# Optimization experiments

Measured on AMD Instinct MI355X. Metric: run time of the kernel, lower is better.

The kernel has to match this reference:

```python
import jax, jax.numpy as jnp
import numpy as np

D_MODEL, H, D_K, D_V = 512, 8, 64, 64
S_Q, S_KV = 2048, 2048


def setup_inputs() -> dict:
    key = jax.random.key(0)
    ks = jax.random.split(key, 11)
    sc = 0.02
    return {
        "embeddings": jax.random.normal(ks[0], (S_Q, D_MODEL), jnp.float32),
        "K": jax.random.normal(ks[1], (S_KV, D_MODEL), jnp.float32),
        "V": jax.random.normal(ks[2], (S_KV, D_MODEL), jnp.float32),
        # per-head projection weights (stacked over heads) + biases
        "Wq": jax.random.normal(ks[3], (H, D_MODEL, D_K), jnp.float32) * sc,
        "bq": jax.random.normal(ks[4], (H, D_K), jnp.float32) * sc,
        "Wk": jax.random.normal(ks[5], (H, D_MODEL, D_K), jnp.float32) * sc,
        "bk": jax.random.normal(ks[6], (H, D_K), jnp.float32) * sc,
        "Wv": jax.random.normal(ks[7], (H, D_MODEL, D_V), jnp.float32) * sc,
        "bv": jax.random.normal(ks[8], (H, D_V), jnp.float32) * sc,
        # final linear: [h*d_v -> d_model]
        "Wo": jax.random.normal(ks[9], (H * D_V, D_MODEL), jnp.float32) * sc,
        "bo": jax.random.normal(ks[10], (D_MODEL,), jnp.float32) * sc,
    }


def reference(embeddings, K, V, Wq, bq, Wk, bk, Wv, bv, Wo, bo):
    # Batched per-head projections (the original loops over h heads; math identical)
    q = jnp.einsum("sd,hdk->hsk", embeddings, Wq) + bq[:, None, :]  # [h, Sq, d_k]
    k = jnp.einsum("td,hdk->htk", K, Wk) + bk[:, None, :]           # [h, Skv, d_k]
    v = jnp.einsum("td,hdv->htv", V, Wv) + bv[:, None, :]           # [h, Skv, d_v]
    scores = jnp.einsum("hsk,htk->hst", q, k) / jnp.sqrt(jnp.asarray(D_K, q.dtype))
    attn = jax.nn.softmax(scores, axis=-1)                           # [h, Sq, Skv]
    out = jnp.einsum("hst,htv->hsv", attn, v)                        # [h, Sq, d_v]
    # torch.cat(results, dim=1): head 0's d_v columns first -> [Sq, h*d_v]
    concat = jnp.transpose(out, (1, 0, 2)).reshape(S_Q, H * D_V)
    return concat @ Wo + bo                                          # [Sq, d_model]
```

## Files before the change

### kernel.cpp

```cpp
#include <hip/hip_runtime.h>

#define SQ 2048
#define DM 512
#define NH 8
#define NSPLIT 4

typedef __bf16 bf16x8 __attribute__((ext_vector_type(8)));
typedef float f32x4 __attribute__((ext_vector_type(4)));
typedef unsigned short us8 __attribute__((ext_vector_type(8)));

__device__ __forceinline__ unsigned short f2bf(float f) {
    unsigned u = __builtin_bit_cast(unsigned, f);
    u += 0x7fffu + ((u >> 16) & 1u);
    return (unsigned short)(u >> 16);
}
__device__ __forceinline__ unsigned short f2bf_trunc(float f) {
    return (unsigned short)(__builtin_bit_cast(unsigned, f) >> 16);
}

__global__ __launch_bounds__(256) void convert_w(
    const float* __restrict__ Wq, const float* __restrict__ Wk, const float* __restrict__ Wv,
    const float* __restrict__ Wo,
    unsigned short* __restrict__ Wt, unsigned short* __restrict__ Wot)
{
    const int b = blockIdx.x, tid = threadIdx.x;
    __shared__ float ld[64 * 68];
    float4* ld4 = reinterpret_cast<float4*>(ld);
    const int rr = tid >> 4, c4 = tid & 15;

    if (b < 192) {
        const int idx = b >> 3;
        const int kt = b & 7;
        const int p = idx >> 3, h = idx & 7;
        const float* src = ((p == 0) ? Wq : (p == 1) ? Wk : Wv)
                         + (size_t)h * 512 * 64 + (size_t)kt * 64 * 64;
        unsigned short* dst = Wt + (size_t)idx * 64 * 512 + kt * 64;
        #pragma unroll
        for (int it = 0; it < 4; it++) {
            int r = rr + 16 * it;
            ld4[r * 17 + c4] = reinterpret_cast<const float4*>(src + (size_t)r * 64)[c4];
        }
        __syncthreads();
        #pragma unroll
        for (int it = 0; it < 2; it++) {
            int slot = tid + it * 256;
            int n = slot >> 3, g = slot & 7;
            us8 o;
            #pragma unroll
            for (int i = 0; i < 8; i++)
                o[i] = f2bf(ld[(g * 8 + i) * 68 + n]);
            *reinterpret_cast<us8*>(dst + (size_t)n * 512 + g * 8) = o;
        }
    } else {
        const int ti = b - 192;
        const int kt = ti >> 3, nt = ti & 7;
        const float* src = Wo + (size_t)kt * 64 * 512 + nt * 64;
        #pragma unroll
        for (int it = 0; it < 4; it++) {
            int r = rr + 16 * it;
            ld4[r * 17 + c4] = reinterpret_cast<const float4*>(src + (size_t)r * 512)[c4];
        }
        __syncthreads();
        #pragma unroll
        for (int it = 0; it < 2; it++) {
            int slot = tid + it * 256;
            int n = slot >> 3, g = slot & 7;
            us8 o;
            #pragma unroll
            for (int i = 0; i < 8; i++)
                o[i] = f2bf(ld[(g * 8 + i) * 68 + n]);
            *reinterpret_cast<us8*>(Wot + (size_t)(nt * 64 + n) * 512 + kt * 64 + g * 8) = o;
        }
    }
}

__global__ __launch_bounds__(256) void qkv_mfma(
    const float* __restrict__ emb, const float* __restrict__ Kin, const float* __restrict__ Vin,
    const unsigned short* __restrict__ Wt,
    const float* __restrict__ bq, const float* __restrict__ bk, const float* __restrict__ bv,
    unsigned short* __restrict__ qo, unsigned short* __restrict__ ko, unsigned short* __restrict__ vo)
{
    const int p = blockIdx.z, h = blockIdx.y, s0 = blockIdx.x * 64;
    const float* X = (p == 0) ? emb : (p == 1) ? Kin : Vin;
    const unsigned short* W = Wt + (size_t)(p * 8 + h) * 64 * 512;
    const float* B = ((p == 0) ? bq : (p == 1) ? bk : bv) + h * 64;

    const int tid = threadIdx.x;
    const int w = tid >> 6, lane = tid & 63, cl = lane & 15, q4 = lane >> 4;
    const int sr = tid >> 3, sg = tid & 7;

    __shared__ unsigned short As[2][64 * 72];
    __shared__ unsigned short Bs[2][64 * 72];

    #pragma unroll
    for (int it = 0; it < 2; it++) {
        int r = sr + 32 * it;
        const float* xr = &X[(size_t)(s0 + r) * 512 + sg * 8];
        float4 f0 = *reinterpret_cast<const float4*>(xr);
        float4 f1 = *reinterpret_cast<const float4*>(xr + 4);
        us8 o;
        o[0] = f2bf(f0.x); o[1] = f2bf(f0.y); o[2] = f2bf(f0.z); o[3] = f2bf(f0.w);
        o[4] = f2bf(f1.x); o[5] = f2bf(f1.y); o[6] = f2bf(f1.z); o[7] = f2bf(f1.w);
        *reinterpret_cast<us8*>(&As[0][r * 72 + sg * 8]) = o;
        *reinterpret_cast<float4*>(&Bs[0][r * 72 + sg * 8]) =
            *reinterpret_cast<const float4*>(&W[(size_t)r * 512 + sg * 8]);
    }

    f32x4 acc[4] = {};

    for (int c = 0; c < 8; c++) {
        __syncthreads();
        const int buf = c & 1;
        const bool more = (c + 1 < 8);
        float4 x0[2], x1[2], br[2];
        if (more) {
            #pragma unroll
            for (int it = 0; it < 2; it++) {
                int r = sr + 32 * it;
                const float* xr = &X[(size_t)(s0 + r) * 512 + (c + 1) * 64 + sg * 8];
                x0[it] = *reinterpret_cast<const float4*>(xr);
                x1[it] = *reinterpret_cast<const float4*>(xr + 4);
                br[it] = *reinterpret_cast<const float4*>(
                    &W[(size_t)r * 512 + (c + 1) * 64 + sg * 8]);
            }
        }

        bf16x8 a0 = *reinterpret_cast<const bf16x8*>(&As[buf][(16 * w + cl) * 72 + q4 * 8]);
        bf16x8 a1 = *reinterpret_cast<const bf16x8*>(&As[buf][(16 * w + cl) * 72 + 32 + q4 * 8]);
        #pragma unroll
        for (int nn = 0; nn < 4; nn++) {
            bf16x8 b0 = *reinterpret_cast<const bf16x8*>(&Bs[buf][(16 * nn + cl) * 72 + q4 * 8]);
            bf16x8 b1 = *reinterpret_cast<const bf16x8*>(&Bs[buf][(16 * nn + cl) * 72 + 32 + q4 * 8]);
            acc[nn] = __builtin_amdgcn_mfma_f32_16x16x32_bf16(a0, b0, acc[nn], 0, 0, 0);
            acc[nn] = __builtin_amdgcn_mfma_f32_16x16x32_bf16(a1, b1, acc[nn], 0, 0, 0);
        }

        if (more) {
            const int nbuf = buf ^ 1;
            #pragma unroll
            for (int it = 0; it < 2; it++) {
                int r = sr + 32 * it;
                us8 o;
                o[0] = f2bf(x0[it].x); o[1] = f2bf(x0[it].y);
                o[2] = f2bf(x0[it].z); o[3] = f2bf(x0[it].w);
                o[4] = f2bf(x1[it].x); o[5] = f2bf(x1[it].y);
                o[6] = f2bf(x1[it].z); o[7] = f2bf(x1[it].w);
                *reinterpret_cast<us8*>(&As[nbuf][r * 72 + sg * 8]) = o;
                *reinterpret_cast<float4*>(&Bs[nbuf][r * 72 + sg * 8]) = br[it];
            }
        }
    }

    if (p == 0) {
        #pragma unroll
        for (int nn = 0; nn < 4; nn++) {
            int col = 16 * nn + cl;
            float bb = B[col];
            #pragma unroll
            for (int r = 0; r < 4; r++)
                qo[((size_t)h * SQ + s0 + 16 * w + q4 * 4 + r) * 64 + col] =
                    f2bf((acc[nn][r] + bb) * 0.125f);
        }
    } else if (p == 1) {
        #pragma unroll
        for (int nn = 0; nn < 4; nn++) {
            int col = 16 * nn + cl;
            float bb = B[col];
            #pragma unroll
            for (int r = 0; r < 4; r++)
                ko[((size_t)h * SQ + s0 + 16 * w + q4 * 4 + r) * 64 + col] =
                    f2bf(acc[nn][r] + bb);
        }
    } else {
        #pragma unroll
        for (int nn = 0; nn < 4; nn++) {
            int col = 16 * nn + cl;
            float bb = B[col];
            ushort4 o;
            o.x = f2bf(acc[nn][0] + bb);
            o.y = f2bf(acc[nn][1] + bb);
            o.z = f2bf(acc[nn][2] + bb);
            o.w = f2bf(acc[nn][3] + bb);
            *reinterpret_cast<ushort4*>(
                vo + ((size_t)h * 64 + col) * SQ + s0 + 16 * w + q4 * 4) = o;
        }
    }
}

#define PW 72

__global__ __launch_bounds__(256) void attn_fwd(
    const unsigned short* __restrict__ qbf,
    const unsigned short* __restrict__ kbf,
    const unsigned short* __restrict__ vbf,
    float* __restrict__ Opart,
    float* __restrict__ lpart)
{
    const int bx = blockIdx.x;
    const int z = bx >> 3, h = bx & 7;
    const int s0 = blockIdx.y * 64;
    const int tid = threadIdx.x;
    const int w = tid >> 6, lane = tid & 63, cl = lane & 15, q4 = lane >> 4;
    const int NT = SQ / 64 / NSPLIT;
    const int t0 = z * NT;

    __shared__ unsigned short Ks[2][64 * PW];
    __shared__ unsigned short Vs[2][64 * PW];
    __shared__ unsigned short Ps[4][16 * PW];

    bf16x8 aq0 = *reinterpret_cast<const bf16x8*>(
        &qbf[((size_t)h * SQ + s0 + 16 * w + cl) * 64 + q4 * 8]);
    bf16x8 aq1 = *reinterpret_cast<const bf16x8*>(
        &qbf[((size_t)h * SQ + s0 + 16 * w + cl) * 64 + 32 + q4 * 8]);

    const int sr = tid >> 3, sg = tid & 7;

    #pragma unroll
    for (int it = 0; it < 2; it++) {
        int r = sr + 32 * it;
        *reinterpret_cast<float4*>(&Ks[0][r * PW + sg * 8]) =
            *reinterpret_cast<const float4*>(&kbf[((size_t)h * SQ + t0 * 64 + r) * 64 + sg * 8]);
        *reinterpret_cast<float4*>(&Vs[0][r * PW + sg * 8]) =
            *reinterpret_cast<const float4*>(&vbf[((size_t)h * 64 + r) * SQ + t0 * 64 + sg * 8]);
    }

    f32x4 o_acc[4] = {};
    float lsum[4] = {};

    for (int tl = 0; tl < NT; tl++) {
        __syncthreads();
        const int buf = tl & 1;
        const bool more = (tl + 1 < NT);
        float4 kr[2], vr[2];
        if (more) {
            #pragma unroll
            for (int it = 0; it < 2; it++) {
                int r = sr + 32 * it;
                kr[it] = *reinterpret_cast<const float4*>(
                    &kbf[((size_t)h * SQ + (t0 + tl + 1) * 64 + r) * 64 + sg * 8]);
                vr[it] = *reinterpret_cast<const float4*>(
                    &vbf[((size_t)h * 64 + r) * SQ + (t0 + tl + 1) * 64 + sg * 8]);
            }
        }

        f32x4 s_acc[4] = {};
        #pragma unroll
        for (int nn = 0; nn < 4; nn++) {
            bf16x8 b0 = *reinterpret_cast<const bf16x8*>(&Ks[buf][(16 * nn + cl) * PW + q4 * 8]);
            bf16x8 b1 = *reinterpret_cast<const bf16x8*>(&Ks[buf][(16 * nn + cl) * PW + 32 + q4 * 8]);
            s_acc[nn] = __builtin_amdgcn_mfma_f32_16x16x32_bf16(aq0, b0, s_acc[nn], 0, 0, 0);
            s_acc[nn] = __builtin_amdgcn_mfma_f32_16x16x32_bf16(aq1, b1, s_acc[nn], 0, 0, 0);
        }

        #pragma unroll
        for (int r = 0; r < 4; r++) {
            #pragma unroll
            for (int nn = 0; nn < 4; nn++) {
                float pv = __expf(s_acc[nn][r]);
                lsum[r] += pv;
                Ps[w][(q4 * 4 + r) * PW + 16 * nn + cl] = f2bf_trunc(pv);
            }
        }
        bf16x8 ap0 = *reinterpret_cast<const bf16x8*>(&Ps[w][cl * PW + q4 * 8]);
        bf16x8 ap1 = *reinterpret_cast<const bf16x8*>(&Ps[w][cl * PW + 32 + q4 * 8]);

        #pragma unroll
        for (int nn = 0; nn < 4; nn++) {
            bf16x8 b0 = *reinterpret_cast<const bf16x8*>(&Vs[buf][(16 * nn + cl) * PW + q4 * 8]);
            bf16x8 b1 = *reinterpret_cast<const bf16x8*>(&Vs[buf][(16 * nn + cl) * PW + 32 + q4 * 8]);
            o_acc[nn] = __builtin_amdgcn_mfma_f32_16x16x32_bf16(ap0, b0, o_acc[nn], 0, 0, 0);
            o_acc[nn] = __builtin_amdgcn_mfma_f32_16x16x32_bf16(ap1, b1, o_acc[nn], 0, 0, 0);
        }

        if (more) {
            const int nbuf = buf ^ 1;
            #pragma unroll
            for (int it = 0; it < 2; it++) {
                int r = sr + 32 * it;
                *reinterpret_cast<float4*>(&Ks[nbuf][r * PW + sg * 8]) = kr[it];
                *reinterpret_cast<float4*>(&Vs[nbuf][r * PW + sg * 8]) = vr[it];
            }
        }
    }

    #pragma unroll
    for (int r = 0; r < 4; r++) {
        float v = lsum[r];
        #pragma unroll
        for (int off = 1; off < 16; off <<= 1) v += __shfl_xor(v, off);
        lsum[r] = v;
    }

    const size_t zb = (size_t)bx;
    if (cl == 0) {
        #pragma unroll
        for (int r = 0; r < 4; r++)
            lpart[zb * SQ + s0 + 16 * w + q4 * 4 + r] = lsum[r];
    }
    #pragma unroll
    for (int nn = 0; nn < 4; nn++)
        #pragma unroll
        for (int r = 0; r < 4; r++)
            Opart[(zb * SQ + s0 + 16 * w + q4 * 4 + r) * 64 + 16 * nn + cl] = o_acc[nn][r];
}

__global__ __launch_bounds__(256) void out_proj(
    const float* __restrict__ Opart, const float* __restrict__ lpart,
    const unsigned short* __restrict__ Wot,
    const float* __restrict__ bo, float* __restrict__ out)
{
    const int s0 = blockIdx.x * 64, n0 = blockIdx.y * 64;
    const int tid = threadIdx.x;
    const int w = tid >> 6, lane = tid & 63, cl = lane & 15, q4 = lane >> 4;
    const int sr = tid >> 3, sg = tid & 7;

    __shared__ unsigned short As[2][64 * 72];
    __shared__ unsigned short Bs[2][64 * 72];
    __shared__ float invL[512];

    #pragma unroll
    for (int k = 0; k < 2; k++) {
        int idx = tid * 2 + k;
        int hh = idx >> 6, ss = idx & 63;
        float l = 0.f;
        #pragma unroll
        for (int z = 0; z < NSPLIT; z++)
            l += lpart[(size_t)(z * 8 + hh) * SQ + s0 + ss];
        invL[idx] = 1.0f / l;
    }
    __syncthreads();

    #pragma unroll
    for (int it = 0; it < 2; it++) {
        int r = sr + 32 * it;
        float o[8] = {};
        #pragma unroll
        for (int z = 0; z < NSPLIT; z++) {
            const float4* pp = reinterpret_cast<const float4*>(
                &Opart[((size_t)(z * 8) * SQ + s0 + r) * 64 + sg * 8]);
            float4 a = pp[0], b = pp[1];
            o[0] += a.x; o[1] += a.y; o[2] += a.z; o[3] += a.w;
            o[4] += b.x; o[5] += b.y; o[6] += b.z; o[7] += b.w;
        }
        float il = invL[r];
        us8 pk;
        #pragma unroll
        for (int i = 0; i < 8; i++) pk[i] = f2bf(o[i] * il);
        *reinterpret_cast<us8*>(&As[0][r * 72 + sg * 8]) = pk;
        *reinterpret_cast<float4*>(&Bs[0][r * 72 + sg * 8]) =
            *reinterpret_cast<const float4*>(&Wot[(size_t)(n0 + r) * 512 + sg * 8]);
    }

    f32x4 acc[4] = {};

    for (int c = 0; c < 8; c++) {
        __syncthreads();
        const int buf = c & 1;
        const bool more = (c + 1 < 8);
        float4 pre[2][NSPLIT][2];
        float4 wr[2];
        if (more) {
            const int hn = c + 1;
            #pragma unroll
            for (int it = 0; it < 2; it++) {
                int r = sr + 32 * it;
                #pragma unroll
                for (int z = 0; z < NSPLIT; z++) {
                    const float4* pp = reinterpret_cast<const float4*>(
                        &Opart[((size_t)(z * 8 + hn) * SQ + s0 + r) * 64 + sg * 8]);
                    pre[it][z][0] = pp[0];
                    pre[it][z][1] = pp[1];
                }
                wr[it] = *reinterpret_cast<const float4*>(
                    &Wot[(size_t)(n0 + r) * 512 + hn * 64 + sg * 8]);
            }
        }

        bf16x8 a0 = *reinterpret_cast<const bf16x8*>(&As[buf][(16 * w + cl) * 72 + q4 * 8]);
        bf16x8 a1 = *reinterpret_cast<const bf16x8*>(&As[buf][(16 * w + cl) * 72 + 32 + q4 * 8]);
        #pragma unroll
        for (int nn = 0; nn < 4; nn++) {
            bf16x8 b0 = *reinterpret_cast<const bf16x8*>(&Bs[buf][(16 * nn + cl) * 72 + q4 * 8]);
            bf16x8 b1 = *reinterpret_cast<const bf16x8*>(&Bs[buf][(16 * nn + cl) * 72 + 32 + q4 * 8]);
            acc[nn] = __builtin_amdgcn_mfma_f32_16x16x32_bf16(a0, b0, acc[nn], 0, 0, 0);
            acc[nn] = __builtin_amdgcn_mfma_f32_16x16x32_bf16(a1, b1, acc[nn], 0, 0, 0);
        }

        if (more) {
            const int nbuf = buf ^ 1;
            const int hn = c + 1;
            #pragma unroll
            for (int it = 0; it < 2; it++) {
                int r = sr + 32 * it;
                float o[8] = {};
                #pragma unroll
                for (int z = 0; z < NSPLIT; z++) {
                    float4 a = pre[it][z][0], b = pre[it][z][1];
                    o[0] += a.x; o[1] += a.y; o[2] += a.z; o[3] += a.w;
                    o[4] += b.x; o[5] += b.y; o[6] += b.z; o[7] += b.w;
                }
                float il = invL[hn * 64 + r];
                us8 pk;
                #pragma unroll
                for (int i = 0; i < 8; i++) pk[i] = f2bf(o[i] * il);
                *reinterpret_cast<us8*>(&As[nbuf][r * 72 + sg * 8]) = pk;
                *reinterpret_cast<float4*>(&Bs[nbuf][r * 72 + sg * 8]) = wr[it];
            }
        }
    }

    #pragma unroll
    for (int nn = 0; nn < 4; nn++) {
        int col = n0 + 16 * nn + cl;
        float bb = bo[col];
        #pragma unroll
        for (int r = 0; r < 4; r++)
            out[(size_t)(s0 + 16 * w + q4 * 4 + r) * DM + col] = acc[nn][r] + bb;
    }
}

extern "C" void kernel_launch(void* const* d_in, const int* in_sizes, int n_in,
                              void* d_out, int out_size, void* d_ws, size_t ws_size,
                              hipStream_t stream) {
    const float* emb = (const float*)d_in[0];
    const float* Kin = (const float*)d_in[1];
    const float* Vin = (const float*)d_in[2];
    const float* Wq  = (const float*)d_in[3];
    const float* bq  = (const float*)d_in[4];
    const float* Wk  = (const float*)d_in[5];
    const float* bk  = (const float*)d_in[6];
    const float* Wv  = (const float*)d_in[7];
    const float* bv  = (const float*)d_in[8];
    const float* Wo  = (const float*)d_in[9];
    const float* bo  = (const float*)d_in[10];
    float* out = (float*)d_out;

    unsigned short* p = (unsigned short*)d_ws;
    unsigned short* Wt  = p; p += (size_t)24 * 64 * 512;
    unsigned short* Wot = p; p += (size_t)512 * 512;
    unsigned short* qbf = p; p += (size_t)NH * SQ * 64;
    unsigned short* kbf = p; p += (size_t)NH * SQ * 64;
    unsigned short* vbf = p; p += (size_t)NH * SQ * 64;
    float* Opart = (float*)p;
    float* lpart = Opart + (size_t)NSPLIT * NH * SQ * 64;

    convert_w<<<256, 256, 0, stream>>>(Wq, Wk, Wv, Wo, Wt, Wot);
    qkv_mfma<<<dim3(32, 8, 3), 256, 0, stream>>>(emb, Kin, Vin, Wt, bq, bk, bv,
                                                 qbf, kbf, vbf);
    attn_fwd<<<dim3(32, 32), 256, 0, stream>>>(qbf, kbf, vbf, Opart, lpart);
    out_proj<<<dim3(32, 8), 256, 0, stream>>>(Opart, lpart, Wot, bo, out);
}
```

Measured before the change: 130.6 us.

## Fuse all stages into one cooperative persistent kernel with grid syncs

```diff
diff --git a/kernel.cpp b/kernel.cpp
--- a/kernel.cpp
+++ b/kernel.cpp
@@ -1,9 +1,12 @@
 #include <hip/hip_runtime.h>
+#include <hip/hip_cooperative_groups.h>
+
+namespace cg = cooperative_groups;
 
 #define SQ 2048
 #define DM 512
 #define NH 8
-#define NSPLIT 4
+#define NZ 2
 
 typedef __bf16 bf16x8 __attribute__((ext_vector_type(8)));
 typedef float f32x4 __attribute__((ext_vector_type(4)));
@@ -18,19 +21,19 @@
     return (unsigned short)(__builtin_bit_cast(unsigned, f) >> 16);
 }
 
-__global__ __launch_bounds__(256) void convert_w(
-    const float* __restrict__ Wq, const float* __restrict__ Wk, const float* __restrict__ Wv,
-    const float* __restrict__ Wo,
-    unsigned short* __restrict__ Wt, unsigned short* __restrict__ Wot)
-{
-    const int b = blockIdx.x, tid = threadIdx.x;
-    __shared__ float ld[64 * 68];
-    float4* ld4 = reinterpret_cast<float4*>(ld);
+__device__ __forceinline__ void phase0(
+    int b, int tid, unsigned char* smem,
+    const float* emb, const float* Kin, const float* Vin,
+    const float* Wq,  const float* Wk,  const float* Wv,  const float* Wo,
+    unsigned short* xe, unsigned short* xk, unsigned short* xv,
+    unsigned short* Wt, unsigned short* Wot)
+{
+    float* ld = (float*)smem;
+    float4* ld4 = (float4*)smem;
     const int rr = tid >> 4, c4 = tid & 15;
 
     if (b < 192) {
-        const int idx = b >> 3;
-        const int kt = b & 7;
+        const int idx = b >> 3, kt = b & 7;
         const int p = idx >> 3, h = idx & 7;
         const float* src = ((p == 0) ? Wq : (p == 1) ? Wk : Wv)
                          + (size_t)h * 512 * 64 + (size_t)kt * 64 * 64;
@@ -51,7 +54,7 @@
                 o[i] = f2bf(ld[(g * 8 + i) * 68 + n]);
             *reinterpret_cast<us8*>(dst + (size_t)n * 512 + g * 8) = o;
         }
-    } else {
+    } else if (b < 256) {
         const int ti = b - 192;
         const int kt = ti >> 3, nt = ti & 7;
         const float* src = Wo + (size_t)kt * 64 * 512 + nt * 64;
@@ -71,168 +74,191 @@
                 o[i] = f2bf(ld[(g * 8 + i) * 68 + n]);
             *reinterpret_cast<us8*>(Wot + (size_t)(nt * 64 + n) * 512 + kt * 64 + g * 8) = o;
         }
-    }
-}
-
-__global__ __launch_bounds__(256) void qkv_mfma(
-    const float* __restrict__ emb, const float* __restrict__ Kin, const float* __restrict__ Vin,
-    const unsigned short* __restrict__ Wt,
-    const float* __restrict__ bq, const float* __restrict__ bk, const float* __restrict__ bv,
-    unsigned short* __restrict__ qo, unsigned short* __restrict__ ko, unsigned short* __restrict__ vo)
-{
-    const int p = blockIdx.z, h = blockIdx.y, s0 = blockIdx.x * 64;
-    const float* X = (p == 0) ? emb : (p == 1) ? Kin : Vin;
+    } else {
+        const int u = b - 256;
+        #pragma unroll
+        for (int k = 0; k < 6; k++) {
+            int o = tid + k * 256;
+            int rl = o >> 6, oc = o & 63;
+            int g = u * 24 + rl;
+            int m = g >> 11, r = g & 2047;
+            const float* src = (m == 0) ? emb : (m == 1) ? Kin : Vin;
+            unsigned short* dst = (m == 0) ? xe : (m == 1) ? xk : xv;
+            const float4* s4 = reinterpret_cast<const float4*>(src + (size_t)r * 512 + oc * 8);
+            float4 f0 = s4[0], f1 = s4[1];
+            us8 oo;
+            oo[0] = f2bf(f0.x); oo[1] = f2bf(f0.y); oo[2] = f2bf(f0.z); oo[3] = f2bf(f0.w);
+            oo[4] = f2bf(f1.x); oo[5] = f2bf(f1.y); oo[6] = f2bf(f1.z); oo[7] = f2bf(f1.w);
+            *reinterpret_cast<us8*>(dst + (size_t)r * 512 + oc * 8) = oo;
+        }
+    }
+}
+
+__device__ __forceinline__ void phase1(
+    int b, int tid, unsigned char* smem,
+    const unsigned short* xe, const unsigned short* xk, const unsigned short* xv,
+    const unsigned short* Wt,
+    const float* bq, const float* bk, const float* bv,
+    unsigned short* qbf, unsigned short* kbf, unsigned short* vbf)
+{
+    const int p = b >> 7, rem = b & 127;
+    const int h = rem >> 4, s0 = (rem & 15) * 128;
+    const unsigned short* X = (p == 0) ? xe : (p == 1) ? xk : xv;
     const unsigned short* W = Wt + (size_t)(p * 8 + h) * 64 * 512;
     const float* B = ((p == 0) ? bq : (p == 1) ? bk : bv) + h * 64;
 
-    const int tid = threadIdx.x;
+    unsigned short* As = (unsigned short*)smem;
+    unsigned short* Bs = (unsigned short*)(smem + 18432);
+
+    const int w = tid >> 6, lane = tid & 63, cl = lane & 15, q4 = lane >> 4;
+
+    float4 ar[4], br[2];
+    #pragma unroll
+    for (int it = 0; it < 4; it++) {
+        int slot = tid + it * 256; int r = slot >> 3, g = slot & 7;
+        ar[it] = *reinterpret_cast<const float4*>(&X[(size_t)(s0 + r) * 512 + g * 8]);
+    }
+    #pragma unroll
+    for (int it = 0; it < 2; it++) {
+        int slot = tid + it * 256; int n = slot >> 3, g = slot & 7;
+        br[it] = *reinterpret_cast<const float4*>(&W[(size_t)n * 512 + g * 8]);
+    }
+
+    f32x4 acc[2][4] = {};
+    for (int c = 0; c < 8; c++) {
+        if (c) __syncthreads();
+        #pragma unroll
+        for (int it = 0; it < 4; it++) {
+            int slot = tid + it * 256; int r = slot >> 3, g = slot & 7;
+            *reinterpret_cast<float4*>(&As[r * 72 + g * 8]) = ar[it];
+        }
+        #pragma unroll
+        for (int it = 0; it < 2; it++) {
+            int slot = tid + it * 256; int n = slot >> 3, g = slot & 7;
+            *reinterpret_cast<float4*>(&Bs[n * 72 + g * 8]) = br[it];
+        }
+        __syncthreads();
+        if (c + 1 < 8) {
+            #pragma unroll
+            for (int it = 0; it < 4; it++) {
+                int slot = tid + it * 256; int r = slot >> 3, g = slot & 7;
+                ar[it] = *reinterpret_cast<const float4*>(
+                    &X[(size_t)(s0 + r) * 512 + (c + 1) * 64 + g * 8]);
+            }
+            #pragma unroll
+            for (int it = 0; it < 2; it++) {
+                int slot = tid + it * 256; int n = slot >> 3, g = slot & 7;
+                br[it] = *reinterpret_cast<const float4*>(
+                    &W[(size_t)n * 512 + (c + 1) * 64 + g * 8]);
+            }
+        }
+        bf16x8 a[2][2];
+        #pragma unroll
+        for (int mi = 0; mi < 2; mi++)
+            #pragma unroll
+            for (int ch = 0; ch < 2; ch++)
+                a[mi][ch] = *reinterpret_cast<const bf16x8*>(
+                    &As[(32 * w + 16 * mi + cl) * 72 + ch * 32 + q4 * 8]);
+        #pragma unroll
+        for (int nn = 0; nn < 4; nn++) {
+            #pragma unroll
+            for (int ch = 0; ch < 2; ch++) {
+                bf16x8 bfr = *reinterpret_cast<const bf16x8*>(
+                    &Bs[(16 * nn + cl) * 72 + ch * 32 + q4 * 8]);
+                #pragma unroll
+                for (int mi = 0; mi < 2; mi++)
+                    acc[mi][nn] = __builtin_amdgcn_mfma_f32_16x16x32_bf16(
+                        a[mi][ch], bfr, acc[mi][nn], 0, 0, 0);
+            }
+        }
+    }
+
+    #pragma unroll
+    for (int mi = 0; mi < 2; mi++) {
+        const int row0 = s0 + 32 * w + 16 * mi + q4 * 4;
+        if (p == 0) {
+            #pragma unroll
+            for (int nn = 0; nn < 4; nn++) {
+                int col = 16 * nn + cl;
+                float bb = B[col];
+                #pragma unroll
+                for (int r = 0; r < 4; r++)
+                    qbf[((size_t)h * SQ + row0 + r) * 64 + col] =
+                        f2bf((acc[mi][nn][r] + bb) * 0.125f);
+            }
+        } else if (p == 1) {
+            #pragma unroll
+            for (int nn = 0; nn < 4; nn++) {
+                int col = 16 * nn + cl;
+                float bb = B[col];
+                #pragma unroll
+                for (int r = 0; r < 4; r++)
+                    kbf[((size_t)h * SQ + row0 + r) * 64 + col] =
+                        f2bf(acc[mi][nn][r] + bb);
+            }
+        } else {
+            #pragma unroll
+            for (int nn = 0; nn < 4; nn++) {
+                int col = 16 * nn + cl;
+                float bb = B[col];
+                ushort4 o;
+                o.x = f2bf(acc[mi][nn][0] + bb);
+                o.y = f2bf(acc[mi][nn][1] + bb);
+                o.z = f2bf(acc[mi][nn][2] + bb);
+                o.w = f2bf(acc[mi][nn][3] + bb);
+                *reinterpret_cast<ushort4*>(vbf + ((size_t)h * 64 + col) * SQ + row0) = o;
+            }
+        }
+    }
+}
+
+__device__ __forceinline__ void phase2(
+    int b, int tid, unsigned char* smem,
+    const unsigned short* qbf, const unsigned short* kbf, const unsigned short* vbf,
+    float* Opart, float* lpart)
+{
+    const int h = b & 7;
+    const int qd = b >> 3;
+    const int z = qd & 1, sbk = qd >> 1;
+    const int s0 = sbk * 64;
+    const int t0 = z * 16;
+    const int NT = 16;
+
+    unsigned short* Ks = (unsigned short*)smem;
+    unsigned short* Vs = (unsigned short*)(smem + 9216);
+    unsigned short* Ps = (unsigned short*)(smem + 18432) + (tid >> 6) * 1152;
+
     const int w = tid >> 6, lane = tid & 63, cl = lane & 15, q4 = lane >> 4;
     const int sr = tid >> 3, sg = tid & 7;
-
-    __shared__ unsigned short As[2][64 * 72];
-    __shared__ unsigned short Bs[2][64 * 72];
-
-    #pragma unroll
-    for (int it = 0; it < 2; it++) {
-        int r = sr + 32 * it;
-        const float* xr = &X[(size_t)(s0 + r) * 512 + sg * 8];
-        float4 f0 = *reinterpret_cast<const float4*>(xr);
-        float4 f1 = *reinterpret_cast<const float4*>(xr + 4);
-        us8 o;
-        o[0] = f2bf(f0.x); o[1] = f2bf(f0.y); o[2] = f2bf(f0.z); o[3] = f2bf(f0.w);
-        o[4] = f2bf(f1.x); o[5] = f2bf(f1.y); o[6] = f2bf(f1.z); o[7] = f2bf(f1.w);
-        *reinterpret_cast<us8*>(&As[0][r * 72 + sg * 8]) = o;
-        *reinterpret_cast<float4*>(&Bs[0][r * 72 + sg * 8]) =
-            *reinterpret_cast<const float4*>(&W[(size_t)r * 512 + sg * 8]);
-    }
-
-    f32x4 acc[4] = {};
-
-    for (int c = 0; c < 8; c++) {
-        __syncthreads();
-        const int buf = c & 1;
-        const bool more = (c + 1 < 8);
-        float4 x0[2], x1[2], br[2];
-        if (more) {
-            #pragma unroll
-            for (int it = 0; it < 2; it++) {
-                int r = sr + 32 * it;
-                const float* xr = &X[(size_t)(s0 + r) * 512 + (c + 1) * 64 + sg * 8];
-                x0[it] = *reinterpret_cast<const float4*>(xr);
-                x1[it] = *reinterpret_cast<const float4*>(xr + 4);
-                br[it] = *reinterpret_cast<const float4*>(
-                    &W[(size_t)r * 512 + (c + 1) * 64 + sg * 8]);
-            }
-        }
-
-        bf16x8 a0 = *reinterpret_cast<const bf16x8*>(&As[buf][(16 * w + cl) * 72 + q4 * 8]);
-        bf16x8 a1 = *reinterpret_cast<const bf16x8*>(&As[buf][(16 * w + cl) * 72 + 32 + q4 * 8]);
-        #pragma unroll
-        for (int nn = 0; nn < 4; nn++) {
-            bf16x8 b0 = *reinterpret_cast<const bf16x8*>(&Bs[buf][(16 * nn + cl) * 72 + q4 * 8]);
-            bf16x8 b1 = *reinterpret_cast<const bf16x8*>(&Bs[buf][(16 * nn + cl) * 72 + 32 + q4 * 8]);
-            acc[nn] = __builtin_amdgcn_mfma_f32_16x16x32_bf16(a0, b0, acc[nn], 0, 0, 0);
-            acc[nn] = __builtin_amdgcn_mfma_f32_16x16x32_bf16(a1, b1, acc[nn], 0, 0, 0);
-        }
-
-        if (more) {
-            const int nbuf = buf ^ 1;
-            #pragma unroll
-            for (int it = 0; it < 2; it++) {
-                int r = sr + 32 * it;
-                us8 o;
-                o[0] = f2bf(x0[it].x); o[1] = f2bf(x0[it].y);
-                o[2] = f2bf(x0[it].z); o[3] = f2bf(x0[it].w);
-                o[4] = f2bf(x1[it].x); o[5] = f2bf(x1[it].y);
-                o[6] = f2bf(x1[it].z); o[7] = f2bf(x1[it].w);
-                *reinterpret_cast<us8*>(&As[nbuf][r * 72 + sg * 8]) = o;
-                *reinterpret_cast<float4*>(&Bs[nbuf][r * 72 + sg * 8]) = br[it];
-            }
-        }
-    }
-
-    if (p == 0) {
-        #pragma unroll
-        for (int nn = 0; nn < 4; nn++) {
-            int col = 16 * nn + cl;
-            float bb = B[col];
-            #pragma unroll
-            for (int r = 0; r < 4; r++)
-                qo[((size_t)h * SQ + s0 + 16 * w + q4 * 4 + r) * 64 + col] =
-                    f2bf((acc[nn][r] + bb) * 0.125f);
-        }
-    } else if (p == 1) {
-        #pragma unroll
-        for (int nn = 0; nn < 4; nn++) {
-            int col = 16 * nn + cl;
-            float bb = B[col];
-            #pragma unroll
-            for (int r = 0; r < 4; r++)
-                ko[((size_t)h * SQ + s0 + 16 * w + q4 * 4 + r) * 64 + col] =
-                    f2bf(acc[nn][r] + bb);
-        }
-    } else {
-        #pragma unroll
-        for (int nn = 0; nn < 4; nn++) {
-            int col = 16 * nn + cl;
-            float bb = B[col];
-            ushort4 o;
-            o.x = f2bf(acc[nn][0] + bb);
-            o.y = f2bf(acc[nn][1] + bb);
-            o.z = f2bf(acc[nn][2] + bb);
-            o.w = f2bf(acc[nn][3] + bb);
-            *reinterpret_cast<ushort4*>(
-                vo + ((size_t)h * 64 + col) * SQ + s0 + 16 * w + q4 * 4) = o;
-        }
-    }
-}
-
-#define PW 72
-
-__global__ __launch_bounds__(256) void attn_fwd(
-    const unsigned short* __restrict__ qbf,
-    const unsigned short* __restrict__ kbf,
-    const unsigned short* __restrict__ vbf,
-    float* __restrict__ Opart,
-    float* __restrict__ lpart)
-{
-    const int bx = blockIdx.x;
-    const int z = bx >> 3, h = bx & 7;
-    const int s0 = blockIdx.y * 64;
-    const int tid = threadIdx.x;
-    const int w = tid >> 6, lane = tid & 63, cl = lane & 15, q4 = lane >> 4;
-    const int NT = SQ / 64 / NSPLIT;
-    const int t0 = z * NT;
-
-    __shared__ unsigned short Ks[2][64 * PW];
-    __shared__ unsigned short Vs[2][64 * PW];
-    __shared__ unsigned short Ps[4][16 * PW];
 
     bf16x8 aq0 = *reinterpret_cast<const bf16x8*>(
         &qbf[((size_t)h * SQ + s0 + 16 * w + cl) * 64 + q4 * 8]);
     bf16x8 aq1 = *reinterpret_cast<const bf16x8*>(
         &qbf[((size_t)h * SQ + s0 + 16 * w + cl) * 64 + 32 + q4 * 8]);
 
-    const int sr = tid >> 3, sg = tid & 7;
-
+    float4 kr[2], vr[2];
     #pragma unroll
     for (int it = 0; it < 2; it++) {
         int r = sr + 32 * it;
-        *reinterpret_cast<float4*>(&Ks[0][r * PW + sg * 8]) =
-            *reinterpret_cast<const float4*>(&kbf[((size_t)h * SQ + t0 * 64 + r) * 64 + sg * 8]);
-        *reinterpret_cast<float4*>(&Vs[0][r * PW + sg * 8]) =
-            *reinterpret_cast<const float4*>(&vbf[((size_t)h * 64 + r) * SQ + t0 * 64 + sg * 8]);
+        kr[it] = *reinterpret_cast<const float4*>(
+            &kbf[((size_t)h * SQ + t0 * 64 + r) * 64 + sg * 8]);
+        vr[it] = *reinterpret_cast<const float4*>(
+            &vbf[((size_t)h * 64 + r) * SQ + t0 * 64 + sg * 8]);
     }
 
     f32x4 o_acc[4] = {};
     float lsum[4] = {};
 
     for (int tl = 0; tl < NT; tl++) {
+        if (tl) __syncthreads();
+        #pragma unroll
+        for (int it = 0; it < 2; it++) {
+            int r = sr + 32 * it;
+            *reinterpret_cast<float4*>(&Ks[r * 72 + sg * 8]) = kr[it];
+            *reinterpret_cast<float4*>(&Vs[r * 72 + sg * 8]) = vr[it];
+        }
         __syncthreads();
-        const int buf = tl & 1;
-        const bool more = (tl + 1 < NT);
-        float4 kr[2], vr[2];
-        if (more) {
+        if (tl + 1 < NT) {
             #pragma unroll
             for (int it = 0; it < 2; it++) {
                 int r = sr + 32 * it;
@@ -246,8 +272,8 @@
         f32x4 s_acc[4] = {};
         #pragma unroll
         for (int nn = 0; nn < 4; nn++) {
-            bf16x8 b0 = *reinterpret_cast<const bf16x8*>(&Ks[buf][(16 * nn + cl) * PW + q4 * 8]);
-            bf16x8 b1 = *reinterpret_cast<const bf16x8*>(&Ks[buf][(16 * nn + cl) * PW + 32 + q4 * 8]);
+            bf16x8 b0 = *reinterpret_cast<const bf16x8*>(&Ks[(16 * nn + cl) * 72 + q4 * 8]);
+            bf16x8 b1 = *reinterpret_cast<const bf16x8*>(&Ks[(16 * nn + cl) * 72 + 32 + q4 * 8]);
             s_acc[nn] = __builtin_amdgcn_mfma_f32_16x16x32_bf16(aq0, b0, s_acc[nn], 0, 0, 0);
             s_acc[nn] = __builtin_amdgcn_mfma_f32_16x16x32_bf16(aq1, b1, s_acc[nn], 0, 0, 0);
         }
@@ -258,29 +284,19 @@
             for (int nn = 0; nn < 4; nn++) {
                 float pv = __expf(s_acc[nn][r]);
                 lsum[r] += pv;
-                Ps[w][(q4 * 4 + r) * PW + 16 * nn + cl] = f2bf_trunc(pv);
-            }
-        }
-        bf16x8 ap0 = *reinterpret_cast<const bf16x8*>(&Ps[w][cl * PW + q4 * 8]);
-        bf16x8 ap1 = *reinterpret_cast<const bf16x8*>(&Ps[w][cl * PW + 32 + q4 * 8]);
+                Ps[(q4 * 4 + r) * 72 + 16 * nn + cl] = f2bf_trunc(pv);
+            }
+        }
+        bf16x8 ap0 = *reinterpret_cast<const bf16x8*>(&Ps[cl * 72 + q4 * 8]);
+        bf16x8 ap1 = *reinterpret_cast<const bf16x8*>(&Ps[cl * 72 + 32 + q4 * 8]);
 
         #pragma unroll
         for (int nn = 0; nn < 4; nn++) {
-            bf16x8 b0 = *reinterpret_cast<const bf16x8*>(&Vs[buf][(16 * nn + cl) * PW + q4 * 8]);
-            bf16x8 b1 = *reinterpret_cast<const bf16x8*>(&Vs[buf][(16 * nn + cl) * PW + 32 + q4 * 8]);
+            bf16x8 b0 = *reinterpret_cast<const bf16x8*>(&Vs[(16 * nn + cl) * 72 + q4 * 8]);
+            bf16x8 b1 = *reinterpret_cast<const bf16x8*>(&Vs[(16 * nn + cl) * 72 + 32 + q4 * 8]);
             o_acc[nn] = __builtin_amdgcn_mfma_f32_16x16x32_bf16(ap0, b0, o_acc[nn], 0, 0, 0);
             o_acc[nn] = __builtin_amdgcn_mfma_f32_16x16x32_bf16(ap1, b1, o_acc[nn], 0, 0, 0);
         }
-
-        if (more) {
-            const int nbuf = buf ^ 1;
-            #pragma unroll
-            for (int it = 0; it < 2; it++) {
-                int r = sr + 32 * it;
-                *reinterpret_cast<float4*>(&Ks[nbuf][r * PW + sg * 8]) = kr[it];
-                *reinterpret_cast<float4*>(&Vs[nbuf][r * PW + sg * 8]) = vr[it];
-            }
-        }
     }
 
     #pragma unroll
@@ -291,7 +307,7 @@
         lsum[r] = v;
     }
 
-    const size_t zb = (size_t)bx;
+    const size_t zb = (size_t)(z * 8 + h);
     if (cl == 0) {
         #pragma unroll
         for (int r = 0; r < 4; r++)
@@ -304,19 +320,18 @@
             Opart[(zb * SQ + s0 + 16 * w + q4 * 4 + r) * 64 + 16 * nn + cl] = o_acc[nn][r];
 }
 
-__global__ __launch_bounds__(256) void out_proj(
-    const float* __restrict__ Opart, const float* __restrict__ lpart,
-    const unsigned short* __restrict__ Wot,
-    const float* __restrict__ bo, float* __restrict__ out)
-{
-    const int s0 = blockIdx.x * 64, n0 = blockIdx.y * 64;
-    const int tid = threadIdx.x;
+__device__ __forceinline__ void phase3(
+    int b, int tid, unsigned char* smem,
+    const float* Opart, const float* lpart,
+    const unsigned short* Wot, const float* bo, float* out)
+{
+    const int s0 = (b >> 3) * 64, n0 = (b & 7) * 64;
+    unsigned short* As = (unsigned short*)smem;
+    unsigned short* Bs = (unsigned short*)(smem + 9216);
+    float* invL = (float*)(smem + 18432);
+
     const int w = tid >> 6, lane = tid & 63, cl = lane & 15, q4 = lane >> 4;
     const int sr = tid >> 3, sg = tid & 7;
-
-    __shared__ unsigned short As[2][64 * 72];
-    __shared__ unsigned short Bs[2][64 * 72];
-    __shared__ float invL[512];
 
     #pragma unroll
     for (int k = 0; k < 2; k++) {
@@ -324,88 +339,45 @@
         int hh = idx >> 6, ss = idx & 63;
         float l = 0.f;
         #pragma unroll
-        for (int z = 0; z < NSPLIT; z++)
+        for (int z = 0; z < NZ; z++)
             l += lpart[(size_t)(z * 8 + hh) * SQ + s0 + ss];
         invL[idx] = 1.0f / l;
     }
     __syncthreads();
 
-    #pragma unroll
-    for (int it = 0; it < 2; it++) {
-        int r = sr + 32 * it;
-        float o[8] = {};
-        #pragma unroll
-        for (int z = 0; z < NSPLIT; z++) {
-            const float4* pp = reinterpret_cast<const float4*>(
-                &Opart[((size_t)(z * 8) * SQ + s0 + r) * 64 + sg * 8]);
-            float4 a = pp[0], b = pp[1];
-            o[0] += a.x; o[1] += a.y; o[2] += a.z; o[3] += a.w;
-            o[4] += b.x; o[5] += b.y; o[6] += b.z; o[7] += b.w;
-        }
-        float il = invL[r];
-        us8 pk;
-        #pragma unroll
-        for (int i = 0; i < 8; i++) pk[i] = f2bf(o[i] * il);
-        *reinterpret_cast<us8*>(&As[0][r * 72 + sg * 8]) = pk;
-        *reinterpret_cast<float4*>(&Bs[0][r * 72 + sg * 8]) =
-            *reinterpret_cast<const float4*>(&Wot[(size_t)(n0 + r) * 512 + sg * 8]);
-    }
-
     f32x4 acc[4] = {};
-
     for (int c = 0; c < 8; c++) {
+        if (c) __syncthreads();
+        #pragma unroll
+        for (int it = 0; it < 2; it++) {
+            int r = sr + 32 * it;
+            float o[8] = {};
+            #pragma unroll
+            for (int z = 0; z < NZ; z++) {
+                const float4* pp = reinterpret_cast<const float4*>(
+                    &Opart[((size_t)(z * 8 + c) * SQ + s0 + r) * 64 + sg * 8]);
+                float4 a = pp[0], b4 = pp[1];
+                o[0] += a.x;  o[1] += a.y;  o[2] += a.z;  o[3] += a.w;
+                o[4] += b4.x; o[5] += b4.y; o[6] += b4.z; o[7] += b4.w;
+            }
+            float il = invL[c * 64 + r];
+            us8 pk;
+            #pragma unroll
+            for (int i = 0; i < 8; i++) pk[i] = f2bf(o[i] * il);
+            *reinterpret_cast<us8*>(&As[r * 72 + sg * 8]) = pk;
+            *reinterpret_cast<float4*>(&Bs[r * 72 + sg * 8]) =
+                *reinterpret_cast<const float4*>(&Wot[(size_t)(n0 + r) * 512 + c * 64 + sg * 8]);
+        }
         __syncthreads();
-        const int buf = c & 1;
-        const bool more = (c + 1 < 8);
-        float4 pre[2][NSPLIT][2];
-        float4 wr[2];
-        if (more) {
-            const int hn = c + 1;
-            #pragma unroll
-            for (int it = 0; it < 2; it++) {
-                int r = sr + 32 * it;
-                #pragma unroll
-                for (int z = 0; z < NSPLIT; z++) {
-                    const float4* pp = reinterpret_cast<const float4*>(
-                        &Opart[((size_t)(z * 8 + hn) * SQ + s0 + r) * 64 + sg * 8]);
-                    pre[it][z][0] = pp[0];
-                    pre[it][z][1] = pp[1];
-                }
-                wr[it] = *reinterpret_cast<const float4*>(
-                    &Wot[(size_t)(n0 + r) * 512 + hn * 64 + sg * 8]);
-            }
-        }
-
-        bf16x8 a0 = *reinterpret_cast<const bf16x8*>(&As[buf][(16 * w + cl) * 72 + q4 * 8]);
-        bf16x8 a1 = *reinterpret_cast<const bf16x8*>(&As[buf][(16 * w + cl) * 72 + 32 + q4 * 8]);
+
+        bf16x8 a0 = *reinterpret_cast<const bf16x8*>(&As[(16 * w + cl) * 72 + q4 * 8]);
+        bf16x8 a1 = *reinterpret_cast<const bf16x8*>(&As[(16 * w + cl) * 72 + 32 + q4 * 8]);
         #pragma unroll
         for (int nn = 0; nn < 4; nn++) {
-            bf16x8 b0 = *reinterpret_cast<const bf16x8*>(&Bs[buf][(16 * nn + cl) * 72 + q4 * 8]);
-            bf16x8 b1 = *reinterpret_cast<const bf16x8*>(&Bs[buf][(16 * nn + cl) * 72 + 32 + q4 * 8]);
+            bf16x8 b0 = *reinterpret_cast<const bf16x8*>(&Bs[(16 * nn + cl) * 72 + q4 * 8]);
+            bf16x8 b1 = *reinterpret_cast<const bf16x8*>(&Bs[(16 * nn + cl) * 72 + 32 + q4 * 8]);
             acc[nn] = __builtin_amdgcn_mfma_f32_16x16x32_bf16(a0, b0, acc[nn], 0, 0, 0);
             acc[nn] = __builtin_amdgcn_mfma_f32_16x16x32_bf16(a1, b1, acc[nn], 0, 0, 0);
-        }
-
-        if (more) {
-            const int nbuf = buf ^ 1;
-            const int hn = c + 1;
-            #pragma unroll
-            for (int it = 0; it < 2; it++) {
-                int r = sr + 32 * it;
-                float o[8] = {};
-                #pragma unroll
-                for (int z = 0; z < NSPLIT; z++) {
-                    float4 a = pre[it][z][0], b = pre[it][z][1];
-                    o[0] += a.x; o[1] += a.y; o[2] += a.z; o[3] += a.w;
-                    o[4] += b.x; o[5] += b.y; o[6] += b.z; o[7] += b.w;
-                }
-                float il = invL[hn * 64 + r];
-                us8 pk;
-                #pragma unroll
-                for (int i = 0; i < 8; i++) pk[i] = f2bf(o[i] * il);
-                *reinterpret_cast<us8*>(&As[nbuf][r * 72 + sg * 8]) = pk;
-                *reinterpret_cast<float4*>(&Bs[nbuf][r * 72 + sg * 8]) = wr[it];
-            }
         }
     }
 
@@ -417,6 +389,65 @@
         for (int r = 0; r < 4; r++)
             out[(size_t)(s0 + 16 * w + q4 * 4 + r) * DM + col] = acc[nn][r] + bb;
     }
+}
+
+__global__ void __launch_bounds__(256, 2) fused_all(
+    const float* emb, const float* Kin, const float* Vin,
+    const float* Wq,  const float* Wk,  const float* Wv,  const float* Wo,
+    const float* bq,  const float* bk,  const float* bv,  const float* bo,
+    unsigned short* xe, unsigned short* xk, unsigned short* xv,
+    unsigned short* Wt, unsigned short* Wot,
+    unsigned short* qbf, unsigned short* kbf, unsigned short* vbf,
+    float* Opart, float* lpart, float* out)
+{
+    __shared__ __align__(16) unsigned char smem[27648];
+    const int b = blockIdx.x, tid = threadIdx.x;
+    cg::grid_group grid = cg::this_grid();
+
+    phase0(b, tid, smem, emb, Kin, Vin, Wq, Wk, Wv, Wo, xe, xk, xv, Wt, Wot);
+    grid.sync();
+    if (b < 384) phase1(b, tid, smem, xe, xk, xv, Wt, bq, bk, bv, qbf, kbf, vbf);
+    grid.sync();
+    phase2(b, tid, smem, qbf, kbf, vbf, Opart, lpart);
+    grid.sync();
+    if (b < 256) phase3(b, tid, smem, Opart, lpart, Wot, bo, out);
+}
+
+__global__ __launch_bounds__(256) void k_phase0(
+    const float* emb, const float* Kin, const float* Vin,
+    const float* Wq, const float* Wk, const float* Wv, const float* Wo,
+    unsigned short* xe, unsigned short* xk, unsigned short* xv,
+    unsigned short* Wt, unsigned short* Wot)
+{
+    __shared__ __align__(16) unsigned char smem[17408];
+    phase0(blockIdx.x, threadIdx.x, smem, emb, Kin, Vin, Wq, Wk, Wv, Wo,
+           xe, xk, xv, Wt, Wot);
+}
+
+__global__ __launch_bounds__(256) void k_phase1(
+    const unsigned short* xe, const unsigned short* xk, const unsigned short* xv,
+    const unsigned short* Wt,
+    const float* bq, const float* bk, const float* bv,
+    unsigned short* qbf, unsigned short* kbf, unsigned short* vbf)
+{
+    __shared__ __align__(16) unsigned char smem[27648];
+    phase1(blockIdx.x, threadIdx.x, smem, xe, xk, xv, Wt, bq, bk, bv, qbf, kbf, vbf);
+}
+
+__global__ __launch_bounds__(256) void k_phase2(
+    const unsigned short* qbf, const unsigned short* kbf, const unsigned short* vbf,
+    float* Opart, float* lpart)
+{
+    __shared__ __align__(16) unsigned char smem[27648];
+    phase2(blockIdx.x, threadIdx.x, smem, qbf, kbf, vbf, Opart, lpart);
+}
+
+__global__ __launch_bounds__(256) void k_phase3(
+    const float* Opart, const float* lpart,
+    const unsigned short* Wot, const float* bo, float* out)
+{
+    __shared__ __align__(16) unsigned char smem[20480];
+    phase3(blockIdx.x, threadIdx.x, smem, Opart, lpart, Wot, bo, out);
 }
 
 extern "C" void kernel_launch(void* const* d_in, const int* in_sizes, int n_in,
@@ -436,17 +467,34 @@
     float* out = (float*)d_out;
 
     unsigned short* p = (unsigned short*)d_ws;
+    unsigned short* xe  = p; p += (size_t)SQ * DM;
+    unsigned short* xk  = p; p += (size_t)SQ * DM;
+    unsigned short* xv  = p; p += (size_t)SQ * DM;
     unsigned short* Wt  = p; p += (size_t)24 * 64 * 512;
     unsigned short* Wot = p; p += (size_t)512 * 512;
     unsigned short* qbf = p; p += (size_t)NH * SQ * 64;
     unsigned short* kbf = p; p += (size_t)NH * SQ * 64;
     unsigned short* vbf = p; p += (size_t)NH * SQ * 64;
     float* Opart = (float*)p;
-    float* lpart = Opart + (size_t)NSPLIT * NH * SQ * 64;
-
-    convert_w<<<256, 256, 0, stream>>>(Wq, Wk, Wv, Wo, Wt, Wot);
-    qkv_mfma<<<dim3(32, 8, 3), 256, 0, stream>>>(emb, Kin, Vin, Wt, bq, bk, bv,
-                                                 qbf, kbf, vbf);
-    attn_fwd<<<dim3(32, 32), 256, 0, stream>>>(qbf, kbf, vbf, Opart, lpart);
-    out_proj<<<dim3(32, 8), 256, 0, stream>>>(Opart, lpart, Wot, bo, out);
-}
+    float* lpart = Opart + (size_t)NZ * NH * SQ * 64;
+
+    void* args[] = {
+        (void*)&emb, (void*)&Kin, (void*)&Vin,
+        (void*)&Wq,  (void*)&Wk,  (void*)&Wv,  (void*)&Wo,
+        (void*)&bq,  (void*)&bk,  (void*)&bv,  (void*)&bo,
+        (void*)&xe,  (void*)&xk,  (void*)&xv,
+        (void*)&Wt,  (void*)&Wot,
+        (void*)&qbf, (void*)&kbf, (void*)&vbf,
+        (void*)&Opart, (void*)&lpart, (void*)&out,
+    };
+    hipError_t e = hipLaunchCooperativeKernel((void*)fused_all, dim3(512), dim3(256),
+                                              args, 0, stream);
+    if (e != hipSuccess) {
+        (void)hipGetLastError();
+        k_phase0<<<512, 256, 0, stream>>>(emb, Kin, Vin, Wq, Wk, Wv, Wo,
+                                          xe, xk, xv, Wt, Wot);
+        k_phase1<<<384, 256, 0, stream>>>(xe, xk, xv, Wt, bq, bk, bv, qbf, kbf, vbf);
+        k_phase2<<<512, 256, 0, stream>>>(qbf, kbf, vbf, Opart, lpart);
+        k_phase3<<<256, 256, 0, stream>>>(Opart, lpart, Wot, bo, out);
+    }
+}
```

After: 377.1 us. 2.89x slower.
